# Optimization experiments

Hardware: AMD Instinct MI355X
Metric: run time of the kernel (lower is better)

The kernel has to match this reference:

```python
import jax, jax.numpy as jnp
import numpy as np

SIGMA = 20.0  # outlier threshold used by FindOutliers
EPS = 1e-8


def setup_inputs() -> dict:
    key = jax.random.key(0)
    k1, k2, k3 = jax.random.split(key, 3)
    B, S, K, N = 2, 2048, 4096, 4096
    x = jax.random.normal(k1, (B, S, K), jnp.float32)
    # inject 8 outlier feature columns (|x| > sigma) so the fp correction path is exercised
    out_cols = jnp.arange(8) * (K // 8)
    x = x.at[:, :, out_cols].multiply(30.0)
    weight = jax.random.normal(k2, (N, K), jnp.float32) * (1.0 / np.sqrt(K))
    bias = jax.random.normal(k3, (N,), jnp.float32) * 0.01
    return {"x": x, "weight": weight, "bias": bias}


def reference(x, weight, bias):
    # x: [B,S,K], weight: [N,K], bias: [N]
    B, S, K = x.shape
    N = weight.shape[0]
    xf = x.reshape(-1, K)  # [M,K]

    # FindOutliers: columns where any activation exceeds sigma (as a fixed-size mask)
    col_mask = jnp.any(jnp.abs(xf) > SIGMA, axis=0)          # [K] bool
    keep = jnp.logical_not(col_mask)

    # weight quantization: zero outlier columns, per-output-row symmetric int8
    w_in = weight * keep[None, :].astype(weight.dtype)        # [N,K]
    q_scale = jnp.max(jnp.abs(w_in), axis=1) / 127.0          # [N]
    q_scale = jnp.maximum(q_scale, EPS)
    q_w = jnp.round(jnp.clip(w_in / q_scale[:, None], -128.0, 127.0)).astype(jnp.int8)

    # per-token (row) activation quantization (FindRowScaleF32)
    row_scale = jnp.max(jnp.abs(xf), axis=1, keepdims=True) / 127.0  # [M,1] fp32
    row_scale = jnp.maximum(row_scale, EPS)
    q_x = jnp.round(jnp.clip(xf / row_scale, -128.0, 127.0)).astype(jnp.int8)

    # int8 GEMM with int32 accumulation, then dequant + bias
    acc = jnp.matmul(q_x.astype(jnp.int32), q_w.T.astype(jnp.int32)).astype(jnp.float32)  # [M,N]
    y = acc * row_scale * q_scale[None, :]

    # fp outlier correction: x[:, ind] @ weight[:, ind].T  (dense masked form, same math)
    x_out = xf * col_mask[None, :].astype(xf.dtype)
    y = y + x_out @ weight.T

    y = y + bias[None, :]
    return y.reshape(B, S, N)
```

## Files before the change

kernel.cpp:

```cpp
#include <hip/hip_runtime.h>
#include <stdint.h>

#define K_DIM 4096
#define N_DIM 4096
#define SIGMA 20.0f
#define EPSQ 1e-8f

typedef __attribute__((ext_vector_type(4))) int i32x4;

#define GLDS16(gp, lp)                                                         \
  __builtin_amdgcn_global_load_lds(                                            \
      (const __attribute__((address_space(1))) unsigned int*)(const void*)(gp),\
      (__attribute__((address_space(3))) unsigned int*)(void*)(lp), 16, 0, 0)

__global__ __launch_bounds__(256) void k_rowquant(
    const float* __restrict__ x, float* __restrict__ row_scale,
    int* __restrict__ mask, int8_t* __restrict__ qx)
{
  const int m = blockIdx.x;
  const int t = threadIdx.x;
  const float4* xr = (const float4*)(x + (size_t)m * K_DIM);
  float4 v[4];
  float amax = 0.0f;
#pragma unroll
  for (int i = 0; i < 4; ++i) {
    v[i] = xr[t + i * 256];
    float a0 = fabsf(v[i].x), a1 = fabsf(v[i].y);
    float a2 = fabsf(v[i].z), a3 = fabsf(v[i].w);
    amax = fmaxf(amax, fmaxf(fmaxf(a0, a1), fmaxf(a2, a3)));
    int kbase = (t + i * 256) * 4;
    if (a0 > SIGMA) mask[kbase + 0] = 1;
    if (a1 > SIGMA) mask[kbase + 1] = 1;
    if (a2 > SIGMA) mask[kbase + 2] = 1;
    if (a3 > SIGMA) mask[kbase + 3] = 1;
  }
#pragma unroll
  for (int off = 32; off > 0; off >>= 1)
    amax = fmaxf(amax, __shfl_down(amax, off, 64));
  __shared__ float smax[4];
  __shared__ float sscale;
  if ((t & 63) == 0) smax[t >> 6] = amax;
  __syncthreads();
  if (t == 0) {
    float ms = fmaxf(fmaxf(smax[0], smax[1]), fmaxf(smax[2], smax[3]));
    float rs = fmaxf(ms / 127.0f, EPSQ);
    sscale = rs;
    row_scale[m] = rs;
  }
  __syncthreads();
  const float rs = sscale;
  uint32_t* qxo = (uint32_t*)(qx + (size_t)m * K_DIM);
#pragma unroll
  for (int i = 0; i < 4; ++i) {
    int q0 = (int)rintf(fminf(fmaxf(v[i].x / rs, -128.0f), 127.0f));
    int q1 = (int)rintf(fminf(fmaxf(v[i].y / rs, -128.0f), 127.0f));
    int q2 = (int)rintf(fminf(fmaxf(v[i].z / rs, -128.0f), 127.0f));
    int q3 = (int)rintf(fminf(fmaxf(v[i].w / rs, -128.0f), 127.0f));
    uint32_t packed = (uint32_t)(q0 & 0xff) | ((uint32_t)(q1 & 0xff) << 8) |
                      ((uint32_t)(q2 & 0xff) << 16) | ((uint32_t)(q3 & 0xff) << 24);
    qxo[t + i * 256] = packed;
  }
}

__global__ __launch_bounds__(256) void k_wquant(
    const float* __restrict__ w, const int* __restrict__ mask,
    float* __restrict__ q_scale, int8_t* __restrict__ qw,
    int* __restrict__ outlist, int* __restrict__ count)
{
  const int n = blockIdx.x;
  const int t = threadIdx.x;
  if (n == 0) {
    for (int kk = t; kk < K_DIM; kk += 256) {
      if (mask[kk]) {
        int idx = atomicAdd(count, 1);
        outlist[idx] = kk;
      }
    }
  }
  const float4* wr = (const float4*)(w + (size_t)n * K_DIM);
  const int4* mr = (const int4*)mask;
  float4 v[4];
  float amax = 0.0f;
#pragma unroll
  for (int i = 0; i < 4; ++i) {
    float4 vv = wr[t + i * 256];
    int4 mm = mr[t + i * 256];
    vv.x = mm.x ? 0.0f : vv.x;
    vv.y = mm.y ? 0.0f : vv.y;
    vv.z = mm.z ? 0.0f : vv.z;
    vv.w = mm.w ? 0.0f : vv.w;
    v[i] = vv;
    amax = fmaxf(amax, fmaxf(fmaxf(fabsf(vv.x), fabsf(vv.y)),
                             fmaxf(fabsf(vv.z), fabsf(vv.w))));
  }
#pragma unroll
  for (int off = 32; off > 0; off >>= 1)
    amax = fmaxf(amax, __shfl_down(amax, off, 64));
  __shared__ float smax[4];
  __shared__ float sscale;
  if ((t & 63) == 0) smax[t >> 6] = amax;
  __syncthreads();
  if (t == 0) {
    float ms = fmaxf(fmaxf(smax[0], smax[1]), fmaxf(smax[2], smax[3]));
    float qs = fmaxf(ms / 127.0f, EPSQ);
    sscale = qs;
    q_scale[n] = qs;
  }
  __syncthreads();
  const float qs = sscale;
  uint32_t* qwo = (uint32_t*)(qw + (size_t)n * K_DIM);
#pragma unroll
  for (int i = 0; i < 4; ++i) {
    int q0 = (int)rintf(fminf(fmaxf(v[i].x / qs, -128.0f), 127.0f));
    int q1 = (int)rintf(fminf(fmaxf(v[i].y / qs, -128.0f), 127.0f));
    int q2 = (int)rintf(fminf(fmaxf(v[i].z / qs, -128.0f), 127.0f));
    int q3 = (int)rintf(fminf(fmaxf(v[i].w / qs, -128.0f), 127.0f));
    uint32_t packed = (uint32_t)(q0 & 0xff) | ((uint32_t)(q1 & 0xff) << 8) |
                      ((uint32_t)(q2 & 0xff) << 16) | ((uint32_t)(q3 & 0xff) << 24);
    qwo[t + i * 256] = packed;
  }
}

__global__ __launch_bounds__(512, 2) void k_gemm(
    const int8_t* __restrict__ qx, const int8_t* __restrict__ qw,
    const float* __restrict__ row_scale, const float* __restrict__ q_scale,
    const float* __restrict__ bias,
    const float* __restrict__ x, const float* __restrict__ w,
    const int* __restrict__ outlist, const int* __restrict__ outcount,
    float* __restrict__ out)
{
  __shared__ int8_t As[4][256 * 64];
  __shared__ int8_t Bs[4][256 * 64];

  const int t = threadIdx.x;
  const int m0 = blockIdx.y * 256;
  const int n0 = blockIdx.x * 256;
  const int lane = t & 63;
  const int wave = t >> 6;
  const int wm = (wave >> 2) * 128;
  const int wn = (wave & 3) * 64;
  const int lrow = lane & 15;
  const int kg = lane >> 4;

  i32x4 acc[8][4] = {};

  const int srow = t >> 2;
  const int sclog = (t & 3) ^ ((srow >> 1) & 3);
  const int8_t* gA = qx + (size_t)(m0 + srow) * K_DIM + sclog * 16;
  const int8_t* gB = qw + (size_t)(n0 + srow) * K_DIM + sclog * 16;

  int offA[8], offB[4];
#pragma unroll
  for (int i = 0; i < 8; ++i) {
    int rA = wm + i * 16 + lrow;
    offA[i] = rA * 64 + ((kg ^ ((rA >> 1) & 3)) * 16);
  }
#pragma unroll
  for (int j = 0; j < 4; ++j) {
    int rB = wn + j * 16 + lrow;
    offB[j] = rB * 64 + ((kg ^ ((rB >> 1) & 3)) * 16);
  }

#define STAGE_A(b, tt) do {                                                    \
    GLDS16(gA + (size_t)(tt) * 64, &As[b][t * 16]);                            \
    GLDS16(gA + (size_t)128 * K_DIM + (size_t)(tt) * 64, &As[b][8192 + t * 16]);\
  } while (0)
#define STAGE_B(b, tt) do {                                                    \
    GLDS16(gB + (size_t)(tt) * 64, &Bs[b][t * 16]);                            \
    GLDS16(gB + (size_t)128 * K_DIM + (size_t)(tt) * 64, &Bs[b][8192 + t * 16]);\
  } while (0)

  STAGE_A(0, 0); STAGE_B(0, 0);
  STAGE_A(1, 1); STAGE_B(1, 1);
  STAGE_A(2, 2); STAGE_B(2, 2);
  asm volatile("s_waitcnt vmcnt(8)" ::: "memory");
  __builtin_amdgcn_s_barrier();
  __builtin_amdgcn_sched_barrier(0);

#pragma unroll 4
  for (int kt = 0; kt < 64; ++kt) {
    const int cur = kt & 3;
    const int nx = (kt + 3) & 3;
    const int ktn = (kt + 3) & 63;
    const int8_t* a = &As[cur][0];
    const int8_t* b = &Bs[cur][0];

    i32x4 af[4], bf[4], af2[4];
#pragma unroll
    for (int i = 0; i < 4; ++i) af[i] = *(const i32x4*)(a + offA[i]);
#pragma unroll
    for (int j = 0; j < 4; ++j) bf[j] = *(const i32x4*)(b + offB[j]);
    STAGE_A(nx, ktn);
    STAGE_B(nx, ktn);

    __builtin_amdgcn_s_setprio(1);
#pragma unroll
    for (int i = 0; i < 4; ++i)
#pragma unroll
      for (int j = 0; j < 4; ++j)
        acc[i][j] = __builtin_amdgcn_mfma_i32_16x16x64_i8(af[i], bf[j], acc[i][j], 0, 0, 0);
#pragma unroll
    for (int i = 0; i < 4; ++i) af2[i] = *(const i32x4*)(a + offA[4 + i]);
#pragma unroll
    for (int i = 0; i < 4; ++i)
#pragma unroll
      for (int j = 0; j < 4; ++j)
        acc[4 + i][j] = __builtin_amdgcn_mfma_i32_16x16x64_i8(af2[i], bf[j], acc[4 + i][j], 0, 0, 0);
    __builtin_amdgcn_s_setprio(0);

    asm volatile("s_waitcnt lgkmcnt(0)" ::: "memory");
    asm volatile("s_waitcnt vmcnt(8)" ::: "memory");
    __builtin_amdgcn_s_barrier();
    __builtin_amdgcn_sched_barrier(0);
  }

#undef STAGE_A
#undef STAGE_B

  __syncthreads();
  float* xsh = (float*)&As[0][0];
  float* wsh = (float*)&Bs[0][0];
  const int cnt = *outcount;
  const int cs = cnt < 8 ? cnt : 8;
#pragma unroll
  for (int u = 0; u < 4; ++u) {
    int idx = t * 4 + u;
    int rr = idx >> 3;
    int oo = idx & 7;
    float xv = 0.0f, wv = 0.0f;
    if (oo < cs) {
      int kcol = outlist[oo];
      xv = x[(size_t)(m0 + rr) * K_DIM + kcol];
      wv = w[(size_t)(n0 + rr) * K_DIM + kcol];
    }
    xsh[rr * 8 + oo] = xv;
    wsh[rr * 8 + oo] = wv;
  }
  __syncthreads();

  float qs[4], bv[4];
  int gn[4];
#pragma unroll
  for (int j = 0; j < 4; ++j) {
    gn[j] = n0 + wn + j * 16 + lrow;
    qs[j] = q_scale[gn[j]];
    bv[j] = bias[gn[j]];
  }

#pragma unroll
  for (int i = 0; i < 8; ++i) {
#pragma unroll
    for (int r = 0; r < 4; ++r) {
      int ml = wm + i * 16 + kg * 4 + r;
      int gm = m0 + ml;
      float rs = row_scale[gm];
      float xvv[8];
#pragma unroll
      for (int o = 0; o < 8; ++o) xvv[o] = xsh[ml * 8 + o];
#pragma unroll
      for (int j = 0; j < 4; ++j) {
        int nl = wn + j * 16 + lrow;
        float corr = 0.0f;
#pragma unroll
        for (int o = 0; o < 8; ++o) corr += xvv[o] * wsh[nl * 8 + o];
        for (int o = 8; o < cnt; ++o)
          corr += x[(size_t)gm * K_DIM + outlist[o]] *
                  w[(size_t)gn[j] * K_DIM + outlist[o]];
        float val = (float)acc[i][j][r] * rs * qs[j] + corr + bv[j];
        out[(size_t)gm * N_DIM + gn[j]] = val;
      }
    }
  }
}

extern "C" void kernel_launch(void* const* d_in, const int* in_sizes, int n_in,
                              void* d_out, int out_size, void* d_ws, size_t ws_size,
                              hipStream_t stream) {
  const float* x = (const float*)d_in[0];
  const float* w = (const float*)d_in[1];
  const float* bias = (const float*)d_in[2];
  float* out = (float*)d_out;
  const int M = in_sizes[0] / K_DIM;

  char* ws = (char*)d_ws;
  int* mask = (int*)(ws);
  int* count = (int*)(ws + 16384);
  int* outlist = (int*)(ws + 20480);
  float* row_scale = (float*)(ws + 36864);
  float* q_scale = (float*)(ws + 53248);
  int8_t* qx = (int8_t*)(ws + 131072);
  int8_t* qw = (int8_t*)(ws + 131072 + (size_t)M * K_DIM);

  hipMemsetAsync(ws, 0, 20480, stream);
  k_rowquant<<<M, 256, 0, stream>>>(x, row_scale, mask, qx);
  k_wquant<<<N_DIM, 256, 0, stream>>>(w, mask, q_scale, qw, outlist, count);
  dim3 grid(N_DIM / 256, M / 256);
  k_gemm<<<grid, dim3(512, 1, 1), 0, stream>>>(qx, qw, row_scale, q_scale, bias,
                                               x, w, outlist, count, out);
}
```

Measured before the change: 249.0 us.

## Double-buffer LDS fragments in registers across k-tiles of the int8 GEMM

Restructures the int8 MFMA main loop into a two-way unrolled body that loads the next k-tile's A/B fragments from LDS into a second register set while the current MFMAs run. The second-half A fragments are also loaded earlier in the iteration. The global-to-LDS wait tightens from vmcnt(8) to vmcnt(4) so the next stage is resident before it is read, which cuts the in-flight global prefetch depth. The aim is to hide LDS read latency behind MFMA work, at the cost of more vector registers and less slack for global loads.

```diff
diff --git a/kernel.cpp b/kernel.cpp
--- a/kernel.cpp
+++ b/kernel.cpp
@@ -173,45 +173,53 @@
   STAGE_A(0, 0); STAGE_B(0, 0);
   STAGE_A(1, 1); STAGE_B(1, 1);
   STAGE_A(2, 2); STAGE_B(2, 2);
-  asm volatile("s_waitcnt vmcnt(8)" ::: "memory");
+  asm volatile("s_waitcnt vmcnt(4)" ::: "memory");
   __builtin_amdgcn_s_barrier();
   __builtin_amdgcn_sched_barrier(0);
 
-#pragma unroll 4
-  for (int kt = 0; kt < 64; ++kt) {
-    const int cur = kt & 3;
-    const int nx = (kt + 3) & 3;
-    const int ktn = (kt + 3) & 63;
-    const int8_t* a = &As[cur][0];
-    const int8_t* b = &Bs[cur][0];
-
-    i32x4 af[4], bf[4], af2[4];
-#pragma unroll
-    for (int i = 0; i < 4; ++i) af[i] = *(const i32x4*)(a + offA[i]);
-#pragma unroll
-    for (int j = 0; j < 4; ++j) bf[j] = *(const i32x4*)(b + offB[j]);
+  i32x4 fA0[4], fB0[4], fA1[4], fB1[4];
+#pragma unroll
+  for (int i = 0; i < 4; ++i) fA0[i] = *(const i32x4*)(&As[0][0] + offA[i]);
+#pragma unroll
+  for (int j = 0; j < 4; ++j) fB0[j] = *(const i32x4*)(&Bs[0][0] + offB[j]);
+
+  auto body = [&](int KT, i32x4 (&pA)[4], i32x4 (&pB)[4],
+                  i32x4 (&nA)[4], i32x4 (&nB)[4]) __attribute__((always_inline)) {
+    const int8_t* aC = &As[KT & 3][0];
+    const int8_t* aN = &As[(KT + 1) & 3][0];
+    const int8_t* bN = &Bs[(KT + 1) & 3][0];
+    const int nx = (KT + 3) & 3;
+    const int ktn = (KT + 3) & 63;
     STAGE_A(nx, ktn);
     STAGE_B(nx, ktn);
-
+    i32x4 a2[4];
+#pragma unroll
+    for (int i = 0; i < 4; ++i) a2[i] = *(const i32x4*)(aC + offA[4 + i]);
     __builtin_amdgcn_s_setprio(1);
 #pragma unroll
     for (int i = 0; i < 4; ++i)
 #pragma unroll
       for (int j = 0; j < 4; ++j)
-        acc[i][j] = __builtin_amdgcn_mfma_i32_16x16x64_i8(af[i], bf[j], acc[i][j], 0, 0, 0);
-#pragma unroll
-    for (int i = 0; i < 4; ++i) af2[i] = *(const i32x4*)(a + offA[4 + i]);
+        acc[i][j] = __builtin_amdgcn_mfma_i32_16x16x64_i8(pA[i], pB[j], acc[i][j], 0, 0, 0);
+#pragma unroll
+    for (int i = 0; i < 4; ++i) nA[i] = *(const i32x4*)(aN + offA[i]);
+#pragma unroll
+    for (int j = 0; j < 4; ++j) nB[j] = *(const i32x4*)(bN + offB[j]);
 #pragma unroll
     for (int i = 0; i < 4; ++i)
 #pragma unroll
       for (int j = 0; j < 4; ++j)
-        acc[4 + i][j] = __builtin_amdgcn_mfma_i32_16x16x64_i8(af2[i], bf[j], acc[4 + i][j], 0, 0, 0);
+        acc[4 + i][j] = __builtin_amdgcn_mfma_i32_16x16x64_i8(a2[i], pB[j], acc[4 + i][j], 0, 0, 0);
     __builtin_amdgcn_s_setprio(0);
-
     asm volatile("s_waitcnt lgkmcnt(0)" ::: "memory");
-    asm volatile("s_waitcnt vmcnt(8)" ::: "memory");
+    asm volatile("s_waitcnt vmcnt(4)" ::: "memory");
     __builtin_amdgcn_s_barrier();
     __builtin_amdgcn_sched_barrier(0);
+  };
+
+  for (int kt = 0; kt < 64; kt += 2) {
+    body(kt,     fA0, fB0, fA1, fB1);
+    body(kt + 1, fA1, fB1, fA0, fB0);
   }
 
 #undef STAGE_A
```

Result: slower. 258.6 us (+3.8%).

## Shrink GEMM tile to 128x256, triple-buffer LDS, raise occupancy to 4 blocks

Applied to the files above, without the earlier changes.

Halves the M tile of the int8 GEMM from 256 to 128 rows, cuts the LDS ring from four stages to three with a prefetch distance of two, and raises launch bounds to four blocks per CU. The K loop is manually unrolled by three with fixed buffer indices, and the epilogue staging is split between x and w loads. The aim is higher occupancy and a grid of 512 blocks instead of 256, for better CU fill and latency hiding. The cost is lower arithmetic intensity per block, more global traffic for B, and a shallower prefetch pipeline.

```diff
diff --git a/kernel.cpp b/kernel.cpp
--- a/kernel.cpp
+++ b/kernel.cpp
@@ -121,7 +121,7 @@
   }
 }
 
-__global__ __launch_bounds__(512, 2) void k_gemm(
+__global__ __launch_bounds__(512, 4) void k_gemm(
     const int8_t* __restrict__ qx, const int8_t* __restrict__ qw,
     const float* __restrict__ row_scale, const float* __restrict__ q_scale,
     const float* __restrict__ bias,
@@ -129,93 +129,78 @@
     const int* __restrict__ outlist, const int* __restrict__ outcount,
     float* __restrict__ out)
 {
-  __shared__ int8_t As[4][256 * 64];
-  __shared__ int8_t Bs[4][256 * 64];
+  __shared__ int8_t As[3][128 * 64];
+  __shared__ int8_t Bs[3][256 * 64];
 
   const int t = threadIdx.x;
-  const int m0 = blockIdx.y * 256;
+  const int m0 = blockIdx.y * 128;
   const int n0 = blockIdx.x * 256;
   const int lane = t & 63;
   const int wave = t >> 6;
-  const int wm = (wave >> 2) * 128;
+  const int wm = (wave >> 2) * 64;
   const int wn = (wave & 3) * 64;
   const int lrow = lane & 15;
   const int kg = lane >> 4;
 
-  i32x4 acc[8][4] = {};
+  i32x4 acc[4][4] = {};
 
   const int srow = t >> 2;
   const int sclog = (t & 3) ^ ((srow >> 1) & 3);
   const int8_t* gA = qx + (size_t)(m0 + srow) * K_DIM + sclog * 16;
   const int8_t* gB = qw + (size_t)(n0 + srow) * K_DIM + sclog * 16;
 
-  int offA[8], offB[4];
-#pragma unroll
-  for (int i = 0; i < 8; ++i) {
+  int offA[4], offB[4];
+#pragma unroll
+  for (int i = 0; i < 4; ++i) {
     int rA = wm + i * 16 + lrow;
     offA[i] = rA * 64 + ((kg ^ ((rA >> 1) & 3)) * 16);
-  }
-#pragma unroll
-  for (int j = 0; j < 4; ++j) {
-    int rB = wn + j * 16 + lrow;
-    offB[j] = rB * 64 + ((kg ^ ((rB >> 1) & 3)) * 16);
-  }
-
-#define STAGE_A(b, tt) do {                                                    \
+    int rB = wn + i * 16 + lrow;
+    offB[i] = rB * 64 + ((kg ^ ((rB >> 1) & 3)) * 16);
+  }
+
+#define STAGE(b, tt) do {                                                      \
     GLDS16(gA + (size_t)(tt) * 64, &As[b][t * 16]);                            \
-    GLDS16(gA + (size_t)128 * K_DIM + (size_t)(tt) * 64, &As[b][8192 + t * 16]);\
-  } while (0)
-#define STAGE_B(b, tt) do {                                                    \
     GLDS16(gB + (size_t)(tt) * 64, &Bs[b][t * 16]);                            \
     GLDS16(gB + (size_t)128 * K_DIM + (size_t)(tt) * 64, &Bs[b][8192 + t * 16]);\
   } while (0)
 
-  STAGE_A(0, 0); STAGE_B(0, 0);
-  STAGE_A(1, 1); STAGE_B(1, 1);
-  STAGE_A(2, 2); STAGE_B(2, 2);
-  asm volatile("s_waitcnt vmcnt(8)" ::: "memory");
+  STAGE(0, 0);
+  STAGE(1, 1);
+  asm volatile("s_waitcnt vmcnt(3)" ::: "memory");
   __builtin_amdgcn_s_barrier();
   __builtin_amdgcn_sched_barrier(0);
 
-#pragma unroll 4
-  for (int kt = 0; kt < 64; ++kt) {
-    const int cur = kt & 3;
-    const int nx = (kt + 3) & 3;
-    const int ktn = (kt + 3) & 63;
-    const int8_t* a = &As[cur][0];
-    const int8_t* b = &Bs[cur][0];
-
-    i32x4 af[4], bf[4], af2[4];
-#pragma unroll
-    for (int i = 0; i < 4; ++i) af[i] = *(const i32x4*)(a + offA[i]);
-#pragma unroll
-    for (int j = 0; j < 4; ++j) bf[j] = *(const i32x4*)(b + offB[j]);
-    STAGE_A(nx, ktn);
-    STAGE_B(nx, ktn);
-
-    __builtin_amdgcn_s_setprio(1);
-#pragma unroll
-    for (int i = 0; i < 4; ++i)
-#pragma unroll
-      for (int j = 0; j < 4; ++j)
-        acc[i][j] = __builtin_amdgcn_mfma_i32_16x16x64_i8(af[i], bf[j], acc[i][j], 0, 0, 0);
-#pragma unroll
-    for (int i = 0; i < 4; ++i) af2[i] = *(const i32x4*)(a + offA[4 + i]);
-#pragma unroll
-    for (int i = 0; i < 4; ++i)
-#pragma unroll
-      for (int j = 0; j < 4; ++j)
-        acc[4 + i][j] = __builtin_amdgcn_mfma_i32_16x16x64_i8(af2[i], bf[j], acc[4 + i][j], 0, 0, 0);
-    __builtin_amdgcn_s_setprio(0);
-
-    asm volatile("s_waitcnt lgkmcnt(0)" ::: "memory");
-    asm volatile("s_waitcnt vmcnt(8)" ::: "memory");
-    __builtin_amdgcn_s_barrier();
-    __builtin_amdgcn_sched_barrier(0);
-  }
-
-#undef STAGE_A
-#undef STAGE_B
+#define KTILE(KT, CUR, NXS) do {                                               \
+    const int8_t* a = &As[CUR][0];                                             \
+    const int8_t* b = &Bs[CUR][0];                                             \
+    STAGE(NXS, ((KT) + 2) & 63);         \
+    i32x4 af[4], bf[4];                                                        \
+    _Pragma("unroll")                                                          \
+    for (int i = 0; i < 4; ++i) af[i] = *(const i32x4*)(a + offA[i]);          \
+    _Pragma("unroll")                                                          \
+    for (int j = 0; j < 4; ++j) bf[j] = *(const i32x4*)(b + offB[j]);          \
+    __builtin_amdgcn_s_setprio(1);                                             \
+    _Pragma("unroll")                                                          \
+    for (int i = 0; i < 4; ++i)                                                \
+      _Pragma("unroll")                                                        \
+      for (int j = 0; j < 4; ++j)                                              \
+        acc[i][j] = __builtin_amdgcn_mfma_i32_16x16x64_i8(af[i], bf[j], acc[i][j], 0, 0, 0); \
+    __builtin_amdgcn_s_setprio(0);                                             \
+    asm volatile("s_waitcnt lgkmcnt(0)" ::: "memory");                         \
+    asm volatile("s_waitcnt vmcnt(3)" ::: "memory");                           \
+    __builtin_amdgcn_s_barrier();                                              \
+    __builtin_amdgcn_sched_barrier(0);                                         \
+  } while (0)
+
+  for (int kt = 0; kt < 63; kt += 3) {
+    KTILE(kt,     0, 2);
+    KTILE(kt + 1, 1, 0);
+    KTILE(kt + 2, 2, 1);
+  }
+  KTILE(63, 0, 2);
+
+#undef KTILE
+#undef STAGE
 
   __syncthreads();
   float* xsh = (float*)&As[0][0];
@@ -223,17 +208,21 @@
   const int cnt = *outcount;
   const int cs = cnt < 8 ? cnt : 8;
 #pragma unroll
+  for (int u = 0; u < 2; ++u) {
+    int idx = t * 2 + u;
+    int rr = idx >> 3;
+    int oo = idx & 7;
+    float xv = 0.0f;
+    if (oo < cs) xv = x[(size_t)(m0 + rr) * K_DIM + outlist[oo]];
+    xsh[rr * 8 + oo] = xv;
+  }
+#pragma unroll
   for (int u = 0; u < 4; ++u) {
     int idx = t * 4 + u;
     int rr = idx >> 3;
     int oo = idx & 7;
-    float xv = 0.0f, wv = 0.0f;
-    if (oo < cs) {
-      int kcol = outlist[oo];
-      xv = x[(size_t)(m0 + rr) * K_DIM + kcol];
-      wv = w[(size_t)(n0 + rr) * K_DIM + kcol];
-    }
-    xsh[rr * 8 + oo] = xv;
+    float wv = 0.0f;
+    if (oo < cs) wv = w[(size_t)(n0 + rr) * K_DIM + outlist[oo]];
     wsh[rr * 8 + oo] = wv;
   }
   __syncthreads();
@@ -248,7 +237,7 @@
   }
 
 #pragma unroll
-  for (int i = 0; i < 8; ++i) {
+  for (int i = 0; i < 4; ++i) {
 #pragma unroll
     for (int r = 0; r < 4; ++r) {
       int ml = wm + i * 16 + kg * 4 + r;
@@ -294,7 +283,7 @@
   hipMemsetAsync(ws, 0, 20480, stream);
   k_rowquant<<<M, 256, 0, stream>>>(x, row_scale, mask, qx);
   k_wquant<<<N_DIM, 256, 0, stream>>>(w, mask, q_scale, qw, outlist, count);
-  dim3 grid(N_DIM / 256, M / 256);
+  dim3 grid(N_DIM / 256, M / 128);
   k_gemm<<<grid, dim3(512, 1, 1), 0, stream>>>(qx, qw, row_scale, q_scale, bias,
                                                x, w, outlist, count, out);
 }
```

Result: slower. 258.9 us (+4.0%).
